# Performance work log

Hardware: AMD Instinct MI355X
Metric: run time of the kernel (lower is better)

## Reference

```python
import jax, jax.numpy as jnp
import numpy as np

DIM = 768
HEADS = 4
NUM_L1 = 16
NUM_L2 = 64
BATCH = 128


def _ln(x, g, b, eps=1e-5):
    m = x.mean(-1, keepdims=True)
    v = x.var(-1, keepdims=True)
    return (x - m) / jnp.sqrt(v + eps) * g + b


def _cluster_attn(x, wq, wk, wv, fcw, fcb, g, b):
    # x: [B, 2, D]; wq/wk/wv: [H*D, D] torch-Linear layout; fcw: [D, H*D]
    B, S, D = x.shape
    H = HEADS
    q = jnp.einsum('bsd,hed->bhse', x, wq.reshape(H, D, D))
    k = jnp.einsum('bsd,hed->bhse', x, wk.reshape(H, D, D))
    v = jnp.einsum('bsd,hed->bhse', x, wv.reshape(H, D, D))
    attn = jax.nn.softmax(jnp.einsum('bhse,bhte->bhst', q, k) / jnp.sqrt(jnp.float32(D)), axis=-1)
    o = jnp.einsum('bhst,bhte->bhse', attn, v)          # [B, H, S, D]
    o = o.transpose(0, 2, 1, 3).reshape(B, S, H * D)     # [B, S, H*D]
    o = o @ fcw.T + fcb                                  # [B, S, D]
    return _ln(o + x, g, b)


def _score_level(tokens, task_p, wq, wk, wv, fcw, fcb, g, b, sg, sb, sw, sbias):
    # tokens: [1, T, D]; task_p: [batch, 1, D]
    bsz = task_p.shape[0]
    T = tokens.shape[1]
    tok = jnp.broadcast_to(tokens, (bsz, T, DIM))
    tp = jnp.broadcast_to(task_p, (bsz, T, DIM))
    combined = jnp.stack([tok, tp], axis=2).reshape(bsz * T, 2, DIM)
    att = _cluster_attn(combined, wq, wk, wv, fcw, fcb, g, b)
    cls = att[:, 0]                                      # [bsz*T, D]
    scores = (_ln(cls, sg, sb) @ sw.T + sbias).reshape(bsz, T)
    return scores


def setup_inputs() -> dict:
    key = jax.random.key(0)
    ks = jax.random.split(key, 32)
    HD = HEADS * DIM

    def n(i, shape, scale):
        return (jax.random.normal(ks[i], shape) * scale).astype(jnp.float32)

    w_std = float(np.sqrt(2.0 / (DIM + DIM)))
    inp = {
        'task_emb': n(0, (BATCH, 1, DIM), 1.0),
        'tokens_l1': n(1, (1, NUM_L1, DIM), 1.0),
        'tokens_l2': n(2, (1, NUM_L2, DIM), 1.0),
        'task_proj_w': n(3, (DIM, DIM), w_std),
        'task_proj_b': jnp.zeros((DIM,), jnp.float32),
        'wq1': n(4, (HD, DIM), w_std), 'wk1': n(5, (HD, DIM), w_std), 'wv1': n(6, (HD, DIM), w_std),
        'fcw1': n(7, (DIM, HD), float(np.sqrt(2.0 / (DIM + HD)))),
        'fcb1': jnp.zeros((DIM,), jnp.float32),
        'lng1': jnp.ones((DIM,), jnp.float32), 'lnb1': jnp.zeros((DIM,), jnp.float32),
        'slng1': jnp.ones((DIM,), jnp.float32), 'slnb1': jnp.zeros((DIM,), jnp.float32),
        'sw1': n(8, (1, DIM), w_std), 'sb1': jnp.zeros((1,), jnp.float32),
        'wq2': n(9, (HD, DIM), w_std), 'wk2': n(10, (HD, DIM), w_std), 'wv2': n(11, (HD, DIM), w_std),
        'fcw2': n(12, (DIM, HD), float(np.sqrt(2.0 / (DIM + HD)))),
        'fcb2': jnp.zeros((DIM,), jnp.float32),
        'lng2': jnp.ones((DIM,), jnp.float32), 'lnb2': jnp.zeros((DIM,), jnp.float32),
        'slng2': jnp.ones((DIM,), jnp.float32), 'slnb2': jnp.zeros((DIM,), jnp.float32),
        'sw2': n(13, (1, DIM), w_std), 'sb2': jnp.zeros((1,), jnp.float32),
    }
    return inp


def reference(task_emb, tokens_l1, tokens_l2, task_proj_w, task_proj_b,
              wq1, wk1, wv1, fcw1, fcb1, lng1, lnb1, slng1, slnb1, sw1, sb1,
              wq2, wk2, wv2, fcw2, fcb2, lng2, lnb2, slng2, slnb2, sw2, sb2):
    # shared task projection (self.task_proj)
    task_p = task_emb @ task_proj_w.T + task_proj_b    # [batch, 1, D]
    l1 = _score_level(tokens_l1, task_p, wq1, wk1, wv1, fcw1, fcb1, lng1, lnb1, slng1, slnb1, sw1, sb1)
    l2 = _score_level(tokens_l2, task_p, wq2, wk2, wv2, fcw2, fcb2, lng2, lnb2, slng2, slnb2, sw2, sb2)
    return jnp.concatenate([l1, l2], axis=-1)           # [batch, NUM_L1 + NUM_L2]
```

## Files before the change

### kernel.cpp

```cpp
#include <hip/hip_runtime.h>
#include <hip/hip_bf16.h>
#include <math.h>

#define DIM 768
#define HEADS 4
#define HDIM 3072
#define BATCH 128

typedef __attribute__((ext_vector_type(8))) short bfrag;
typedef __attribute__((ext_vector_type(4))) float f32x4;

struct GemmDesc {
    const float* A;
    const float* B;
    const float* bias;
    float* C;
    int lda, ldb, ldc;
    int M, N, K;
    int blockBase;
    int nTiles;
};
#define MAXD 12
struct GemmBatch { GemmDesc d[MAXD]; int nDesc; };

__device__ inline short f2bf(float f) {
    union { __hip_bfloat16 h; short s; } u;
    u.h = __float2bfloat16(f);
    return u.s;
}

__global__ __launch_bounds__(256, 4) void gemm_bf16(GemmBatch batch)
{
    __shared__ __attribute__((aligned(16))) short Asl[24 * 512];

    int bid = blockIdx.x;
    int di = 0;
    while (di + 1 < batch.nDesc && bid >= batch.d[di + 1].blockBase) ++di;
    const GemmDesc g = batch.d[di];
    int lb = bid - g.blockBase;
    int mt = lb / g.nTiles;
    int nt = lb - mt * g.nTiles;
    const int m0 = mt * 16, n0 = nt * 256;
    const int lda = g.lda, ldb = g.ldb;
    const float* __restrict__ A = g.A;
    const float* __restrict__ B = g.B;

    const int tid = threadIdx.x;
    const int lane = tid & 63;
    const int w = tid >> 6;

#pragma unroll
    for (int i = 0; i < 6; ++i) {
        int gI = tid + 256 * i;
        int ks = gI >> 6, l = gI & 63;
        const float* src = A + (long)(m0 + (l & 15)) * lda + ks * 32 + ((l >> 4) << 3);
        float4 v0 = *(const float4*)src;
        float4 v1 = *(const float4*)(src + 4);
        short4 s0, s1;
        s0.x = f2bf(v0.x); s0.y = f2bf(v0.y); s0.z = f2bf(v0.z); s0.w = f2bf(v0.w);
        s1.x = f2bf(v1.x); s1.y = f2bf(v1.y); s1.z = f2bf(v1.z); s1.w = f2bf(v1.w);
        *(short4*)&Asl[gI * 8]     = s0;
        *(short4*)&Asl[gI * 8 + 4] = s1;
    }
    __syncthreads();

    const float* Bb = B + (long)(n0 + (w << 6) + (lane & 15)) * ldb + ((lane >> 4) << 3);

    f32x4 acc[4];
#pragma unroll
    for (int s = 0; s < 4; ++s) acc[s] = (f32x4){0.f, 0.f, 0.f, 0.f};

    float4 P[4][2], Q[4][2];

    auto LD = [&](float4 (&S)[4][2], int ks) {
#pragma unroll
        for (int s = 0; s < 4; ++s) {
            const float* p = Bb + (long)(s * 16) * ldb + ks * 32;
            S[s][0] = *(const float4*)p;
            S[s][1] = *(const float4*)(p + 4);
        }
    };
    auto STEP = [&](float4 (&S)[4][2], int ks) {
        bfrag af = *(const bfrag*)&Asl[(ks << 9) + (lane << 3)];
#pragma unroll
        for (int s = 0; s < 4; ++s) {
            bfrag bf;
            bf[0] = f2bf(S[s][0].x); bf[1] = f2bf(S[s][0].y);
            bf[2] = f2bf(S[s][0].z); bf[3] = f2bf(S[s][0].w);
            bf[4] = f2bf(S[s][1].x); bf[5] = f2bf(S[s][1].y);
            bf[6] = f2bf(S[s][1].z); bf[7] = f2bf(S[s][1].w);
            acc[s] = __builtin_amdgcn_mfma_f32_16x16x32_bf16(af, bf, acc[s], 0, 0, 0);
        }
    };

    LD(P, 0); LD(Q, 1);
#pragma unroll
    for (int ks = 0; ks < 24; ks += 2) {
        STEP(P, ks);
        if (ks + 2 < 24) LD(P, ks + 2);
        STEP(Q, ks + 1);
        if (ks + 3 < 24) LD(Q, ks + 3);
    }

    const int gq = lane >> 4;
    const int cn = lane & 15;
#pragma unroll
    for (int s = 0; s < 4; ++s) {
        int n = n0 + (w << 6) + (s << 4) + cn;
        float bv = g.bias ? g.bias[n] : 0.f;
#pragma unroll
        for (int r = 0; r < 4; ++r) {
            int m = m0 + (gq << 2) + r;
            g.C[(long)m * g.ldc + n] = acc[s][r] + bv;
        }
    }
}

struct ScoreDesc {
    const float *tok_q, *tok_k, *k_task, *U_tok, *U_task, *tokens;
    const float *fcb, *lng, *lnb, *slng, *slnb, *sw, *sbias;
    int T, outOff, blockBase, pad;
};
struct ScoreBatch { ScoreDesc d[2]; };

__device__ inline void block_reduce2(float& a, float& b, float* redA, float* redB, int tid)
{
    int lane = tid & 63, wave = tid >> 6;
#pragma unroll
    for (int off = 32; off; off >>= 1) {
        a += __shfl_down(a, off);
        b += __shfl_down(b, off);
    }
    if (lane == 0) { redA[wave] = a; redB[wave] = b; }
    __syncthreads();
    a = redA[0] + redA[1] + redA[2] + redA[3];
    b = redB[0] + redB[1] + redB[2] + redB[3];
    __syncthreads();
}

__global__ __launch_bounds__(256) void score_kernel(ScoreBatch batch, float* __restrict__ out)
{
    const int si = (blockIdx.x >= batch.d[1].blockBase) ? 1 : 0;
    const ScoreDesc g = batch.d[si];
    const int bid = blockIdx.x - g.blockBase;
    const int T = g.T;
    const int b = bid / T;
    const int t = bid - b * T;
    const int tid = threadIdx.x;
    const int lane = tid & 63;
    const int wave = tid >> 6;

    __shared__ float coef[HEADS][2];
    __shared__ float redA[4], redB[4];

    {
        const float4* q4  = (const float4*)(g.tok_q  + (long)t * HDIM + wave * DIM);
        const float4* kt4 = (const float4*)(g.tok_k  + (long)t * HDIM + wave * DIM);
        const float4* kb4 = (const float4*)(g.k_task + (long)b * HDIM + wave * DIM);
        float s00 = 0.f, s01 = 0.f;
#pragma unroll
        for (int j = 0; j < 3; ++j) {
            int idx = lane + 64 * j;
            float4 qv = q4[idx], kt = kt4[idx], kb = kb4[idx];
            s00 += qv.x * kt.x + qv.y * kt.y + qv.z * kt.z + qv.w * kt.w;
            s01 += qv.x * kb.x + qv.y * kb.y + qv.z * kb.z + qv.w * kb.w;
        }
#pragma unroll
        for (int off = 32; off; off >>= 1) {
            s00 += __shfl_down(s00, off);
            s01 += __shfl_down(s01, off);
        }
        if (lane == 0) {
            const float scale = 0.03608439182435161f;
            float x0 = s00 * scale, x1 = s01 * scale;
            float mx = fmaxf(x0, x1);
            float e0 = expf(x0 - mx), e1 = expf(x1 - mx);
            float inv = 1.f / (e0 + e1);
            coef[wave][0] = e0 * inv;
            coef[wave][1] = e1 * inv;
        }
    }
    __syncthreads();

    const float c00 = coef[0][0], c01 = coef[0][1];
    const float c10 = coef[1][0], c11 = coef[1][1];
    const float c20 = coef[2][0], c21 = coef[2][1];
    const float c30 = coef[3][0], c31 = coef[3][1];

    float r[3];
    float sum = 0.f, sq = 0.f;
    const float* Ut = g.U_tok  + (long)t * HDIM;
    const float* Ub = g.U_task + (long)b * HDIM;
#pragma unroll
    for (int j = 0; j < 3; ++j) {
        int d = tid + j * 256;
        float v = g.fcb[d] + g.tokens[(long)t * DIM + d];
        v += c00 * Ut[d]           + c01 * Ub[d];
        v += c10 * Ut[DIM + d]     + c11 * Ub[DIM + d];
        v += c20 * Ut[2 * DIM + d] + c21 * Ub[2 * DIM + d];
        v += c30 * Ut[3 * DIM + d] + c31 * Ub[3 * DIM + d];
        r[j] = v;
        sum += v;
        sq += v * v;
    }
    block_reduce2(sum, sq, redA, redB, tid);
    float mean = sum * (1.f / DIM);
    float var = sq * (1.f / DIM) - mean * mean;
    float inv = rsqrtf(var + 1e-5f);

    float y[3];
    float sum2 = 0.f, sq2 = 0.f;
#pragma unroll
    for (int j = 0; j < 3; ++j) {
        int d = tid + j * 256;
        float v = (r[j] - mean) * inv * g.lng[d] + g.lnb[d];
        y[j] = v;
        sum2 += v;
        sq2 += v * v;
    }
    block_reduce2(sum2, sq2, redA, redB, tid);
    float mean2 = sum2 * (1.f / DIM);
    float var2 = sq2 * (1.f / DIM) - mean2 * mean2;
    float inv2 = rsqrtf(var2 + 1e-5f);

    float partial = 0.f, dummy = 0.f;
#pragma unroll
    for (int j = 0; j < 3; ++j) {
        int d = tid + j * 256;
        float c = (y[j] - mean2) * inv2 * g.slng[d] + g.slnb[d];
        partial += c * g.sw[d];
    }
    block_reduce2(partial, dummy, redA, redB, tid);
    if (tid == 0) out[(long)b * 80 + g.outOff + t] = partial + g.sbias[0];
}

extern "C" void kernel_launch(void* const* d_in, const int* in_sizes, int n_in,
                              void* d_out, int out_size, void* d_ws, size_t ws_size,
                              hipStream_t stream)
{
    const float* task_emb    = (const float*)d_in[0];
    const float* tokens_l1   = (const float*)d_in[1];
    const float* tokens_l2   = (const float*)d_in[2];
    const float* task_proj_w = (const float*)d_in[3];
    const float* task_proj_b = (const float*)d_in[4];

    const float* wq1  = (const float*)d_in[5];
    const float* wk1  = (const float*)d_in[6];
    const float* wv1  = (const float*)d_in[7];
    const float* fcw1 = (const float*)d_in[8];
    const float* fcb1 = (const float*)d_in[9];
    const float* lng1 = (const float*)d_in[10];
    const float* lnb1 = (const float*)d_in[11];
    const float* slng1= (const float*)d_in[12];
    const float* slnb1= (const float*)d_in[13];
    const float* sw1  = (const float*)d_in[14];
    const float* sb1  = (const float*)d_in[15];

    const float* wq2  = (const float*)d_in[16];
    const float* wk2  = (const float*)d_in[17];
    const float* wv2  = (const float*)d_in[18];
    const float* fcw2 = (const float*)d_in[19];
    const float* fcb2 = (const float*)d_in[20];
    const float* lng2 = (const float*)d_in[21];
    const float* lnb2 = (const float*)d_in[22];
    const float* slng2= (const float*)d_in[23];
    const float* slnb2= (const float*)d_in[24];
    const float* sw2  = (const float*)d_in[25];
    const float* sb2  = (const float*)d_in[26];

    float* out = (float*)d_out;

    float* ws = (float*)d_ws;
    float* task_p   = ws;
    float* tq1      = task_p   +  98304;
    float* tk1      = tq1      +  49152;
    float* tv1      = tk1      +  49152;
    float* ut1      = tv1      +  49152;
    float* tq2      = ut1      +  49152;
    float* tk2      = tq2      + 196608;
    float* tv2      = tk2      + 196608;
    float* ut2      = tv2      + 196608;
    float* ktask1   = ut2      + 196608;
    float* vtask1   = ktask1   + 393216;
    float* utask1   = vtask1   + 393216;
    float* ktask2   = utask1   + 393216;
    float* vtask2   = ktask2   + 393216;
    float* utask2   = vtask2   + 393216;

    auto mkDesc = [](const float* A, int lda, const float* B, int ldb,
                     const float* bias, float* C, int ldc,
                     int M, int N, int K, int base) {
        GemmDesc g;
        g.A = A; g.B = B; g.bias = bias; g.C = C;
        g.lda = lda; g.ldb = ldb; g.ldc = ldc;
        g.M = M; g.N = N; g.K = K;
        g.blockBase = base; g.nTiles = N / 256;
        return g;
    };
    auto blocksOf = [](int M, int N) { return (M / 16) * (N / 256); };

    {
        GemmBatch ba; int base = 0, nd = 0;
        ba.d[nd++] = mkDesc(task_emb, DIM, task_proj_w, DIM, task_proj_b,
                            task_p, DIM, BATCH, DIM, DIM, base);
        base += blocksOf(BATCH, DIM);
        const float* tA[2] = { tokens_l1, tokens_l2 };
        int tT[2] = { 16, 64 };
        const float* tW[2][3] = { { wq1, wk1, wv1 }, { wq2, wk2, wv2 } };
        float* tC[2][3] = { { tq1, tk1, tv1 }, { tq2, tk2, tv2 } };
        for (int l = 0; l < 2; ++l)
            for (int w = 0; w < 3; ++w) {
                ba.d[nd++] = mkDesc(tA[l], DIM, tW[l][w], DIM, nullptr,
                                    tC[l][w], HDIM, tT[l], HDIM, DIM, base);
                base += blocksOf(tT[l], HDIM);
            }
        ba.nDesc = nd;
        gemm_bf16<<<dim3(base), dim3(256), 0, stream>>>(ba);
    }

    {
        GemmBatch bb; int base = 0, nd = 0;
        const float* kw[2] = { wk1, wk2 };
        const float* vw[2] = { wv1, wv2 };
        float* kc[2] = { ktask1, ktask2 };
        float* vc[2] = { vtask1, vtask2 };
        for (int l = 0; l < 2; ++l) {
            bb.d[nd++] = mkDesc(task_p, DIM, kw[l], DIM, nullptr,
                                kc[l], HDIM, BATCH, HDIM, DIM, base);
            base += blocksOf(BATCH, HDIM);
            bb.d[nd++] = mkDesc(task_p, DIM, vw[l], DIM, nullptr,
                                vc[l], HDIM, BATCH, HDIM, DIM, base);
            base += blocksOf(BATCH, HDIM);
        }
        const float* fw[2] = { fcw1, fcw2 };
        float* tv[2] = { tv1, tv2 };
        float* ut[2] = { ut1, ut2 };
        int tT[2] = { 16, 64 };
        for (int l = 0; l < 2; ++l)
            for (int h = 0; h < HEADS; ++h) {
                bb.d[nd++] = mkDesc(tv[l] + h * DIM, HDIM, fw[l] + h * DIM, HDIM,
                                    nullptr, ut[l] + h * DIM, HDIM,
                                    tT[l], DIM, DIM, base);
                base += blocksOf(tT[l], DIM);
            }
        bb.nDesc = nd;
        gemm_bf16<<<dim3(base), dim3(256), 0, stream>>>(bb);
    }

    {
        GemmBatch bc; int base = 0, nd = 0;
        const float* fw[2] = { fcw1, fcw2 };
        float* vt[2] = { vtask1, vtask2 };
        float* utk[2] = { utask1, utask2 };
        for (int l = 0; l < 2; ++l)
            for (int h = 0; h < HEADS; ++h) {
                bc.d[nd++] = mkDesc(vt[l] + h * DIM, HDIM, fw[l] + h * DIM, HDIM,
                                    nullptr, utk[l] + h * DIM, HDIM,
                                    BATCH, DIM, DIM, base);
                base += blocksOf(BATCH, DIM);
            }
        bc.nDesc = nd;
        gemm_bf16<<<dim3(base), dim3(256), 0, stream>>>(bc);
    }

    {
        ScoreBatch sb;
        sb.d[0].tok_q = tq1; sb.d[0].tok_k = tk1; sb.d[0].k_task = ktask1;
        sb.d[0].U_tok = ut1; sb.d[0].U_task = utask1; sb.d[0].tokens = tokens_l1;
        sb.d[0].fcb = fcb1; sb.d[0].lng = lng1; sb.d[0].lnb = lnb1;
        sb.d[0].slng = slng1; sb.d[0].slnb = slnb1; sb.d[0].sw = sw1; sb.d[0].sbias = sb1;
        sb.d[0].T = 16; sb.d[0].outOff = 0; sb.d[0].blockBase = 0; sb.d[0].pad = 0;
        sb.d[1].tok_q = tq2; sb.d[1].tok_k = tk2; sb.d[1].k_task = ktask2;
        sb.d[1].U_tok = ut2; sb.d[1].U_task = utask2; sb.d[1].tokens = tokens_l2;
        sb.d[1].fcb = fcb2; sb.d[1].lng = lng2; sb.d[1].lnb = lnb2;
        sb.d[1].slng = slng2; sb.d[1].slnb = slnb2; sb.d[1].sw = sw2; sb.d[1].sbias = sb2;
        sb.d[1].T = 64; sb.d[1].outOff = 16; sb.d[1].blockBase = BATCH * 16; sb.d[1].pad = 0;
        score_kernel<<<dim3(BATCH * 16 + BATCH * 64), dim3(256), 0, stream>>>(sb, out);
    }
}
```

Measured before the change: 285.2 us.

## Restructure GEMM to stage weight strip in LDS and stream all rows

The batched GEMM kernel now assigns each block a 32-column strip of the weight matrix, converts the whole strip (K=768) to bf16 in shared memory once, and streams every row of the activation matrix (up to 128) from global memory. Previously each block held a 16-row A tile and re-read 256 weight columns, so weights were fetched from global memory and converted M/16 times. The change is meant to cut redundant weight traffic and conversion work. In exchange it uses fewer, smaller blocks (128 threads), more accumulator registers, and a non-unrolled K loop, which may lower occupancy and latency hiding.

```diff
diff --git a/kernel.cpp b/kernel.cpp
--- a/kernel.cpp
+++ b/kernel.cpp
@@ -16,9 +16,9 @@
     const float* bias;
     float* C;
     int lda, ldb, ldc;
-    int M, N, K;
+    int M, N;
     int blockBase;
-    int nTiles;
+    int nStrips;
 };
 #define MAXD 12
 struct GemmBatch { GemmDesc d[MAXD]; int nDesc; };
@@ -29,19 +29,18 @@
     return u.s;
 }
 
-__global__ __launch_bounds__(256, 4) void gemm_bf16(GemmBatch batch)
+__global__ __launch_bounds__(128) void gemm_w(GemmBatch batch)
 {
-    __shared__ __attribute__((aligned(16))) short Asl[24 * 512];
+    __shared__ __attribute__((aligned(16))) short Bsl[24576];
 
     int bid = blockIdx.x;
     int di = 0;
     while (di + 1 < batch.nDesc && bid >= batch.d[di + 1].blockBase) ++di;
     const GemmDesc g = batch.d[di];
-    int lb = bid - g.blockBase;
-    int mt = lb / g.nTiles;
-    int nt = lb - mt * g.nTiles;
-    const int m0 = mt * 16, n0 = nt * 256;
+    const int nt = bid - g.blockBase;
+    const int n0 = nt * 32;
     const int lda = g.lda, ldb = g.ldb;
+    const int F = g.M >> 4;
     const float* __restrict__ A = g.A;
     const float* __restrict__ B = g.B;
 
@@ -49,71 +48,77 @@
     const int lane = tid & 63;
     const int w = tid >> 6;
 
-#pragma unroll
-    for (int i = 0; i < 6; ++i) {
-        int gI = tid + 256 * i;
-        int ks = gI >> 6, l = gI & 63;
-        const float* src = A + (long)(m0 + (l & 15)) * lda + ks * 32 + ((l >> 4) << 3);
-        float4 v0 = *(const float4*)src;
-        float4 v1 = *(const float4*)(src + 4);
-        short4 s0, s1;
-        s0.x = f2bf(v0.x); s0.y = f2bf(v0.y); s0.z = f2bf(v0.z); s0.w = f2bf(v0.w);
-        s1.x = f2bf(v1.x); s1.y = f2bf(v1.y); s1.z = f2bf(v1.z); s1.w = f2bf(v1.w);
-        *(short4*)&Asl[gI * 8]     = s0;
-        *(short4*)&Asl[gI * 8 + 4] = s1;
+    {
+        const int ls = tid & 63;
+        const int nf = w;
+        const float* Bp = B + (long)(n0 + nf * 16 + (ls & 15)) * ldb + ((ls >> 4) << 3);
+#pragma unroll
+        for (int i = 0; i < 24; ++i) {
+            float4 v0 = *(const float4*)(Bp + i * 32);
+            float4 v1 = *(const float4*)(Bp + i * 32 + 4);
+            short4 s0, s1;
+            s0.x = f2bf(v0.x); s0.y = f2bf(v0.y); s0.z = f2bf(v0.z); s0.w = f2bf(v0.w);
+            s1.x = f2bf(v1.x); s1.y = f2bf(v1.y); s1.z = f2bf(v1.z); s1.w = f2bf(v1.w);
+            int gI = tid + 128 * i;
+            *(short4*)&Bsl[gI * 8]     = s0;
+            *(short4*)&Bsl[gI * 8 + 4] = s1;
+        }
     }
     __syncthreads();
 
-    const float* Bb = B + (long)(n0 + (w << 6) + (lane & 15)) * ldb + ((lane >> 4) << 3);
-
-    f32x4 acc[4];
-#pragma unroll
-    for (int s = 0; s < 4; ++s) acc[s] = (f32x4){0.f, 0.f, 0.f, 0.f};
-
-    float4 P[4][2], Q[4][2];
-
-    auto LD = [&](float4 (&S)[4][2], int ks) {
-#pragma unroll
-        for (int s = 0; s < 4; ++s) {
-            const float* p = Bb + (long)(s * 16) * ldb + ks * 32;
-            S[s][0] = *(const float4*)p;
-            S[s][1] = *(const float4*)(p + 4);
-        }
+    const float* Ab = A + (long)(lane & 15) * lda + ((lane >> 4) << 3);
+
+    f32x4 acc[8];
+#pragma unroll
+    for (int mf = 0; mf < 8; ++mf) acc[mf] = (f32x4){0.f, 0.f, 0.f, 0.f};
+
+    float4 P[8][2], Q[8][2];
+
+    auto LDA_ = [&](float4 (&S)[8][2], int ks) {
+#pragma unroll
+        for (int mf = 0; mf < 8; ++mf)
+            if (mf < F) {
+                const float* p = Ab + (long)(mf * 16) * lda + ks * 32;
+                S[mf][0] = *(const float4*)p;
+                S[mf][1] = *(const float4*)(p + 4);
+            }
     };
-    auto STEP = [&](float4 (&S)[4][2], int ks) {
-        bfrag af = *(const bfrag*)&Asl[(ks << 9) + (lane << 3)];
-#pragma unroll
-        for (int s = 0; s < 4; ++s) {
-            bfrag bf;
-            bf[0] = f2bf(S[s][0].x); bf[1] = f2bf(S[s][0].y);
-            bf[2] = f2bf(S[s][0].z); bf[3] = f2bf(S[s][0].w);
-            bf[4] = f2bf(S[s][1].x); bf[5] = f2bf(S[s][1].y);
-            bf[6] = f2bf(S[s][1].z); bf[7] = f2bf(S[s][1].w);
-            acc[s] = __builtin_amdgcn_mfma_f32_16x16x32_bf16(af, bf, acc[s], 0, 0, 0);
-        }
+    auto STEP_ = [&](float4 (&S)[8][2], int ks) {
+        bfrag bw = *(const bfrag*)&Bsl[((ks * 2 + w) * 64 + lane) * 8];
+#pragma unroll
+        for (int mf = 0; mf < 8; ++mf)
+            if (mf < F) {
+                bfrag af;
+                af[0] = f2bf(S[mf][0].x); af[1] = f2bf(S[mf][0].y);
+                af[2] = f2bf(S[mf][0].z); af[3] = f2bf(S[mf][0].w);
+                af[4] = f2bf(S[mf][1].x); af[5] = f2bf(S[mf][1].y);
+                af[6] = f2bf(S[mf][1].z); af[7] = f2bf(S[mf][1].w);
+                acc[mf] = __builtin_amdgcn_mfma_f32_16x16x32_bf16(af, bw, acc[mf], 0, 0, 0);
+            }
     };
 
-    LD(P, 0); LD(Q, 1);
-#pragma unroll
+    LDA_(P, 0); LDA_(Q, 1);
+#pragma unroll 1
     for (int ks = 0; ks < 24; ks += 2) {
-        STEP(P, ks);
-        if (ks + 2 < 24) LD(P, ks + 2);
-        STEP(Q, ks + 1);
-        if (ks + 3 < 24) LD(Q, ks + 3);
+        STEP_(P, ks);
+        if (ks + 2 < 24) LDA_(P, ks + 2);
+        STEP_(Q, ks + 1);
+        if (ks + 3 < 24) LDA_(Q, ks + 3);
     }
 
     const int gq = lane >> 4;
     const int cn = lane & 15;
-#pragma unroll
-    for (int s = 0; s < 4; ++s) {
-        int n = n0 + (w << 6) + (s << 4) + cn;
-        float bv = g.bias ? g.bias[n] : 0.f;
-#pragma unroll
-        for (int r = 0; r < 4; ++r) {
-            int m = m0 + (gq << 2) + r;
-            g.C[(long)m * g.ldc + n] = acc[s][r] + bv;
-        }
-    }
+    const int n = n0 + w * 16 + cn;
+    const float bv = g.bias ? g.bias[n] : 0.f;
+#pragma unroll
+    for (int mf = 0; mf < 8; ++mf)
+        if (mf < F) {
+#pragma unroll
+            for (int r = 0; r < 4; ++r) {
+                int m = mf * 16 + gq * 4 + r;
+                g.C[(long)m * g.ldc + n] = acc[mf][r] + bv;
+            }
+        }
 }
 
 struct ScoreDesc {
@@ -289,21 +294,20 @@
 
     auto mkDesc = [](const float* A, int lda, const float* B, int ldb,
                      const float* bias, float* C, int ldc,
-                     int M, int N, int K, int base) {
+                     int M, int N, int base) {
         GemmDesc g;
         g.A = A; g.B = B; g.bias = bias; g.C = C;
         g.lda = lda; g.ldb = ldb; g.ldc = ldc;
-        g.M = M; g.N = N; g.K = K;
-        g.blockBase = base; g.nTiles = N / 256;
+        g.M = M; g.N = N;
+        g.blockBase = base; g.nStrips = N / 32;
         return g;
     };
-    auto blocksOf = [](int M, int N) { return (M / 16) * (N / 256); };
 
     {
         GemmBatch ba; int base = 0, nd = 0;
         ba.d[nd++] = mkDesc(task_emb, DIM, task_proj_w, DIM, task_proj_b,
-                            task_p, DIM, BATCH, DIM, DIM, base);
-        base += blocksOf(BATCH, DIM);
+                            task_p, DIM, BATCH, DIM, base);
+        base += DIM / 32;
         const float* tA[2] = { tokens_l1, tokens_l2 };
         int tT[2] = { 16, 64 };
         const float* tW[2][3] = { { wq1, wk1, wv1 }, { wq2, wk2, wv2 } };
@@ -311,11 +315,11 @@
         for (int l = 0; l < 2; ++l)
             for (int w = 0; w < 3; ++w) {
                 ba.d[nd++] = mkDesc(tA[l], DIM, tW[l][w], DIM, nullptr,
-                                    tC[l][w], HDIM, tT[l], HDIM, DIM, base);
-                base += blocksOf(tT[l], HDIM);
+                                    tC[l][w], HDIM, tT[l], HDIM, base);
+                base += HDIM / 32;
             }
         ba.nDesc = nd;
-        gemm_bf16<<<dim3(base), dim3(256), 0, stream>>>(ba);
+        gemm_w<<<dim3(base), dim3(128), 0, stream>>>(ba);
     }
 
     {
@@ -326,11 +330,11 @@
         float* vc[2] = { vtask1, vtask2 };
         for (int l = 0; l < 2; ++l) {
             bb.d[nd++] = mkDesc(task_p, DIM, kw[l], DIM, nullptr,
-                                kc[l], HDIM, BATCH, HDIM, DIM, base);
-            base += blocksOf(BATCH, HDIM);
+                                kc[l], HDIM, BATCH, HDIM, base);
+            base += HDIM / 32;
             bb.d[nd++] = mkDesc(task_p, DIM, vw[l], DIM, nullptr,
-                                vc[l], HDIM, BATCH, HDIM, DIM, base);
-            base += blocksOf(BATCH, HDIM);
+                                vc[l], HDIM, BATCH, HDIM, base);
+            base += HDIM / 32;
         }
         const float* fw[2] = { fcw1, fcw2 };
         float* tv[2] = { tv1, tv2 };
@@ -340,11 +344,11 @@
             for (int h = 0; h < HEADS; ++h) {
                 bb.d[nd++] = mkDesc(tv[l] + h * DIM, HDIM, fw[l] + h * DIM, HDIM,
                                     nullptr, ut[l] + h * DIM, HDIM,
-                                    tT[l], DIM, DIM, base);
-                base += blocksOf(tT[l], DIM);
+                                    tT[l], DIM, base);
+                base += DIM / 32;
             }
         bb.nDesc = nd;
-        gemm_bf16<<<dim3(base), dim3(256), 0, stream>>>(bb);
+        gemm_w<<<dim3(base), dim3(128), 0, stream>>>(bb);
     }
 
     {
@@ -356,11 +360,11 @@
             for (int h = 0; h < HEADS; ++h) {
                 bc.d[nd++] = mkDesc(vt[l] + h * DIM, HDIM, fw[l] + h * DIM, HDIM,
                                     nullptr, utk[l] + h * DIM, HDIM,
-                                    BATCH, DIM, DIM, base);
-                base += blocksOf(BATCH, DIM);
+                                    BATCH, DIM, base);
+                base += DIM / 32;
             }
         bc.nDesc = nd;
-        gemm_bf16<<<dim3(base), dim3(256), 0, stream>>>(bc);
+        gemm_w<<<dim3(base), dim3(128), 0, stream>>>(bc);
     }
 
     {
```

New measurement: 426.3 us. 1.49x slower.
